# Kernel tuning notes

Measured on AMD Instinct MI355X. Metric: run time of the kernel, lower is better.

## Reference

```python
import jax, jax.numpy as jnp
import numpy as np

# static config (matches init_kwargs)
E = 1280          # n_embed
L = 4             # n_layer
NH = 16           # n_heads
D = E // NH       # head_dim = 80
M = 5120          # n_mlp
O = 2048          # n_output_embed
MS = 2            # spatial_merge_size
NGPS = 48         # sqrt(num_position_embeddings)
GRID_T, GRID_H, GRID_W = 1, 32, 32
N_IMG = 2
SPP = GRID_T * GRID_H * GRID_W   # 1024 tokens per image
S = N_IMG * SPP                  # 2048 total tokens
H4 = E * MS * MS                 # merger hidden = 5120
IN_PATCH = 3 * 2 * 16 * 16       # 1536
DS_IDX = [1, 2]


def _ln(x, w, b, eps=1e-6):
    m = x.mean(-1, keepdims=True)
    v = ((x - m) ** 2).mean(-1, keepdims=True)
    return (x - m) / jnp.sqrt(v + eps) * w + b


def _pos_embed_interp(pos_emb):
    # bilinear interpolation of the 48x48 learned grid to GRID_HxGRID_W, per image
    hi = jnp.linspace(0.0, NGPS - 1.0, GRID_H)
    wi = jnp.linspace(0.0, NGPS - 1.0, GRID_W)
    hf = hi.astype(jnp.int32); wf = wi.astype(jnp.int32)
    hc = jnp.minimum(hf + 1, NGPS - 1); wc = jnp.minimum(wf + 1, NGPS - 1)
    dh = hi - hf; dw = wi - wf
    idx = [(hf[:, None] * NGPS + wf[None]).ravel(), (hf[:, None] * NGPS + wc[None]).ravel(),
           (hc[:, None] * NGPS + wf[None]).ravel(), (hc[:, None] * NGPS + wc[None]).ravel()]
    wts = [((1 - dh)[:, None] * (1 - dw)[None]).ravel(), ((1 - dh)[:, None] * dw[None]).ravel(),
           (dh[:, None] * (1 - dw)[None]).ravel(), (dh[:, None] * dw[None]).ravel()]
    pe = sum(pos_emb[i] * w[:, None] for i, w in zip(idx, wts))  # [h*w, E]
    pe = jnp.tile(pe, (GRID_T, 1))
    # spatial-merge permutation: (t, h/m, m, w/m, m) -> (t, h/m, w/m, m, m)
    pe = pe.reshape(GRID_T, GRID_H // MS, MS, GRID_W // MS, MS, E).transpose(0, 1, 3, 2, 4, 5).reshape(-1, E)
    return jnp.tile(pe, (N_IMG, 1))  # [S, E]


def _rotary_freqs():
    dim = D // 2  # VisionRotaryEmbedding dim = 40
    inv = 1.0 / (10000.0 ** (jnp.arange(0, dim, 2, dtype=jnp.float32) / dim))  # [D//4]
    hp = jnp.broadcast_to(jnp.arange(GRID_H)[:, None], (GRID_H, GRID_W))
    hp = hp.reshape(GRID_H // MS, MS, GRID_W // MS, MS).transpose(0, 2, 1, 3).ravel()
    wp = jnp.broadcast_to(jnp.arange(GRID_W)[None, :], (GRID_H, GRID_W))
    wp = wp.reshape(GRID_H // MS, MS, GRID_W // MS, MS).transpose(0, 2, 1, 3).ravel()
    pos = jnp.stack([hp, wp], -1)            # [h*w, 2]
    pos = jnp.tile(pos, (GRID_T, 1))
    pos = jnp.tile(pos, (N_IMG, 1))          # [S, 2]
    table = jnp.arange(max(GRID_H, GRID_W), dtype=jnp.float32)[:, None] * inv[None]  # [G, D//4]
    return table[pos].reshape(S, -1)         # [S, D//2] (h-freqs || w-freqs)


def _rope(t, cos, sin):
    # t: [S, NH, D]; cos/sin: [S, 1, D]; applied in float32 as in the source
    t1, t2 = jnp.split(t, 2, axis=-1)
    rot = jnp.concatenate([-t2, t1], -1)
    return (t.astype(jnp.float32) * cos + rot.astype(jnp.float32) * sin).astype(t.dtype)


def _attn(x, qkv_w, qkv_b, pw, pb, cos, sin, mask):
    qkv = (x @ qkv_w.T + qkv_b).reshape(S, 3, NH, D)
    q, k, v = qkv[:, 0], qkv[:, 1], qkv[:, 2]
    q = _rope(q, cos, sin)
    k = _rope(k, cos, sin)
    scores = jnp.einsum('shd,thd->hst', q, k) / np.sqrt(D).astype(np.float32) + mask
    p = jax.nn.softmax(scores.astype(jnp.float32), axis=-1).astype(q.dtype)
    o = jnp.einsum('hst,thd->shd', p, v).reshape(S, E)
    return o @ pw.T + pb


def _merger(x, ln_w, ln_b, f1w, f1b, f2w, f2b, post):
    if post:
        x = _ln(x.reshape(-1, H4), ln_w, ln_b)
    else:
        x = _ln(x, ln_w, ln_b).reshape(-1, H4)
    h = jax.nn.gelu(x @ f1w.T + f1b, approximate=False)  # nn.GELU() exact
    return h @ f2w.T + f2b


def setup_inputs() -> dict:
    key = jax.random.key(0)
    ks = iter(jax.random.split(key, 24))
    n = lambda s: jax.random.normal(next(ks), s, dtype=jnp.float32) * 0.02
    return {
        'x': jax.random.normal(next(ks), (S, IN_PATCH), dtype=jnp.float32),
        'patch_w': n((E, IN_PATCH)), 'patch_b': jnp.zeros((E,), jnp.float32),
        'pos_emb': n((NGPS * NGPS, E)),
        'ln1_w': jnp.ones((L, E), jnp.float32), 'ln1_b': jnp.zeros((L, E), jnp.float32),
        'ln2_w': jnp.ones((L, E), jnp.float32), 'ln2_b': jnp.zeros((L, E), jnp.float32),
        'qkv_w': n((L, 3 * E, E)), 'qkv_b': jnp.zeros((L, 3 * E), jnp.float32),
        'attn_proj_w': n((L, E, E)), 'attn_proj_b': jnp.zeros((L, E), jnp.float32),
        'fc1_w': n((L, M, E)), 'fc1_b': jnp.zeros((L, M), jnp.float32),
        'fc2_w': n((L, E, M)), 'fc2_b': jnp.zeros((L, E), jnp.float32),
        'm_ln_w': jnp.ones((E,), jnp.float32), 'm_ln_b': jnp.zeros((E,), jnp.float32),
        'm_fc1_w': n((H4, H4)), 'm_fc1_b': jnp.zeros((H4,), jnp.float32),
        'm_fc2_w': n((O, H4)), 'm_fc2_b': jnp.zeros((O,), jnp.float32),
        'ds_ln_w': jnp.ones((2, H4), jnp.float32), 'ds_ln_b': jnp.zeros((2, H4), jnp.float32),
        'ds_fc1_w': n((2, H4, H4)), 'ds_fc1_b': jnp.zeros((2, H4), jnp.float32),
        'ds_fc2_w': n((2, O, H4)), 'ds_fc2_b': jnp.zeros((2, O), jnp.float32),
    }


def reference(x, patch_w, patch_b, pos_emb, ln1_w, ln1_b, ln2_w, ln2_b,
              qkv_w, qkv_b, attn_proj_w, attn_proj_b, fc1_w, fc1_b, fc2_w, fc2_b,
              m_ln_w, m_ln_b, m_fc1_w, m_fc1_b, m_fc2_w, m_fc2_b,
              ds_ln_w, ds_ln_b, ds_fc1_w, ds_fc1_b, ds_fc2_w, ds_fc2_b):
    # patch embed (Conv3d with kernel==stride == per-patch linear)
    h = x @ patch_w.T + patch_b                      # [S, E]
    h = h + _pos_embed_interp(pos_emb)
    freqs = _rotary_freqs()                          # [S, D//2]
    cos = jnp.concatenate([jnp.cos(freqs)] * 2, -1)[:, None, :]  # [S,1,D]
    sin = jnp.concatenate([jnp.sin(freqs)] * 2, -1)[:, None, :]
    img = jnp.arange(S) // SPP                       # cu_seqlens block-diagonal mask
    mask = jnp.where(img[:, None] == img[None, :], 0.0, jnp.finfo(jnp.float32).min)
    ds_feats = []
    for l in range(L):
        h = h + _attn(_ln(h, ln1_w[l], ln1_b[l]), qkv_w[l], qkv_b[l],
                      attn_proj_w[l], attn_proj_b[l], cos, sin, mask)
        hn = _ln(h, ln2_w[l], ln2_b[l])
        h = h + (jax.nn.gelu(hn @ fc1_w[l].T + fc1_b[l], approximate=True) @ fc2_w[l].T + fc2_b[l])
        if l in DS_IDX:
            j = DS_IDX.index(l)
            ds_feats.append(_merger(h, ds_ln_w[j], ds_ln_b[j], ds_fc1_w[j], ds_fc1_b[j],
                                    ds_fc2_w[j], ds_fc2_b[j], post=True))
    main = _merger(h, m_ln_w, m_ln_b, m_fc1_w, m_fc1_b, m_fc2_w, m_fc2_b, post=False)
    return jnp.stack([main] + ds_feats, 0)           # [3, S//4, O]
```

## Files before the change

kernel.cpp:

```cpp
#include <hip/hip_runtime.h>
#include <hip/hip_bf16.h>
#include <cstdio>
#include <cstdint>

#define E_    1280
#define L_    4
#define NH_   16
#define D_    80
#define DP_   96
#define MLP_  5120
#define O_    2048
#define S_    2048
#define H4_   5120
#define INP_  1536

typedef __attribute__((ext_vector_type(4))) float f32x4;
typedef __attribute__((ext_vector_type(8))) short short8v;
typedef __attribute__((ext_vector_type(4))) short short4v;

__device__ __forceinline__ short f2bf(float f){
  uint32_t u = __float_as_uint(f);
  uint32_t r = (u + 0x7FFFu + ((u >> 16) & 1u)) >> 16;
  return (short)r;
}
__device__ __forceinline__ float bf2f(short s){
  return __uint_as_float(((uint32_t)(uint16_t)s) << 16);
}
__device__ __forceinline__ float gelu_tanh(float x){
  const float z = 0.7978845608028654f*(x + 0.044715f*x*x*x);
  const float e = __expf(2.f*z);
  return 0.5f*x*(1.f + (e-1.f)/(e+1.f));
}
__device__ __forceinline__ float gelu_erf(float x){
  return 0.5f*x*(1.f + erff(x*0.7071067811865476f));
}
__device__ __forceinline__ void token_hw(int t, int& hc, int& wc){
  hc = ((t>>1)&1) + ((t>>6)<<1);
  wc = (t&1)      + (((t>>2)&15)<<1);
}

__device__ __forceinline__ void gload16(const short* g, short* l){
  __builtin_amdgcn_global_load_lds((const __attribute__((address_space(1))) void*)g,
                                   (__attribute__((address_space(3))) void*)l, 16, 0, 0);
}

__global__ __launch_bounds__(256)
void cvt_k(const float* __restrict__ src, short* __restrict__ dst, long long n)
{
  const long long stride = (long long)gridDim.x*256*8;
  for (long long i = ((long long)blockIdx.x*256 + threadIdx.x)*8; i < n; i += stride){
    float4 v0 = *(const float4*)(src+i);
    float4 v1 = *(const float4*)(src+i+4);
    short8v w;
    w[0]=f2bf(v0.x); w[1]=f2bf(v0.y); w[2]=f2bf(v0.z); w[3]=f2bf(v0.w);
    w[4]=f2bf(v1.x); w[5]=f2bf(v1.y); w[6]=f2bf(v1.z); w[7]=f2bf(v1.w);
    *(short8v*)(dst+i) = w;
  }
}

struct Gemm2P {
  const short* A; const short* B; void* C;
  const float* bias;
  short* part;
  int lda, ldb, ldc, M, N, K;
  float scale;
  long long aOffH, aOffI, bOffH, bOffI, cOffH, cOffI;
  int nImg, kSplit;
};

template<int EPI, bool RES, bool CF32, bool SPLIT>
__global__ __launch_bounds__(256)
void gemm2_k(Gemm2P p)
{
  __shared__ short As[3][4096];
  __shared__ short Bs[3][4096];

  int z = blockIdx.z, ks = 0;
  if constexpr (SPLIT){ ks = z % p.kSplit; z /= p.kSplit; }
  const int hI = z / p.nImg, iI = z % p.nImg;
  const long long aB = (long long)hI*p.aOffH + (long long)iI*p.aOffI;
  const long long bB = (long long)hI*p.bOffH + (long long)iI*p.bOffI;
  const long long cB = (long long)hI*p.cOffH + (long long)iI*p.cOffI;

  const int nwg = gridDim.x*gridDim.y;
  const int orig = blockIdx.y*gridDim.x + blockIdx.x;
  const int q8 = nwg >> 3, r8 = nwg & 7;
  const int xcd = orig & 7, oidx = orig >> 3;
  const int wg = (xcd < r8 ? xcd*(q8+1) : r8*(q8+1) + (xcd-r8)*q8) + oidx;
  const int nt = wg % gridDim.x, mt = wg / gridDim.x;

  const int tid = threadIdx.x, lane = tid & 63, wv = tid >> 6;

  const int sr = lane >> 2;
  const int sc = (lane & 3) * 8;
  const int Kp  = SPLIT ? p.K / p.kSplit : p.K;
  const int kBeg = SPLIT ? ks * Kp : 0;
  int ra0 = mt*128 + (wv*2+0)*16 + sr; if (ra0 >= p.M) ra0 = p.M-1;
  int ra1 = mt*128 + (wv*2+1)*16 + sr; if (ra1 >= p.M) ra1 = p.M-1;
  int rb0 = nt*128 + (wv*2+0)*16 + sr; if (rb0 >= p.N) rb0 = p.N-1;
  int rb1 = nt*128 + (wv*2+1)*16 + sr; if (rb1 >= p.N) rb1 = p.N-1;
  const short* pa0 = p.A + aB + (long long)ra0*p.lda + sc + kBeg;
  const short* pa1 = p.A + aB + (long long)ra1*p.lda + sc + kBeg;
  const short* pb0 = p.B + bB + (long long)rb0*p.ldb + sc + kBeg;
  const short* pb1 = p.B + bB + (long long)rb1*p.ldb + sc + kBeg;
  const int so0 = (wv*2+0)*512;
  const int so1 = (wv*2+1)*512;

  const int fr = lane & 15, fo = (lane >> 4) * 8;
  const int wr = (wv >> 1) * 64, wc = (wv & 1) * 64;

  f32x4 acc[4][4] = {};

  auto stage = [&](int buf, int t){
    const int k0 = t << 5;
    gload16(pa0 + k0, &As[buf][so0]);
    gload16(pa1 + k0, &As[buf][so1]);
    gload16(pb0 + k0, &Bs[buf][so0]);
    gload16(pb1 + k0, &Bs[buf][so1]);
  };

  const int ntile = Kp >> 5;
  stage(0, 0);
  if (ntile > 1) stage(1, 1);
  for (int t = 0; t < ntile; t++){
    const int cur = t % 3;
    if (t + 1 < ntile) { asm volatile("s_waitcnt vmcnt(4)" ::: "memory"); }
    else               { asm volatile("s_waitcnt vmcnt(0)" ::: "memory"); }
    __builtin_amdgcn_s_barrier();
    asm volatile("" ::: "memory");
    short8v a[4], b[4];
    #pragma unroll
    for (int i=0;i<4;i++){
      a[i] = *(const short8v*)&As[cur][(wr + i*16 + fr)*32 + fo];
      b[i] = *(const short8v*)&Bs[cur][(wc + i*16 + fr)*32 + fo];
    }
    if (t + 2 < ntile) stage((t+2)%3, t+2);
    #pragma unroll
    for (int i=0;i<4;i++)
      #pragma unroll
      for (int j=0;j<4;j++)
        acc[i][j] = __builtin_amdgcn_mfma_f32_16x16x32_bf16(a[i], b[j], acc[i][j], 0, 0, 0);
  }

  #pragma unroll
  for (int i=0;i<4;i++){
    #pragma unroll
    for (int j=0;j<4;j++){
      #pragma unroll
      for (int r=0;r<4;r++){
        const int row = mt*128 + wr + i*16 + (lane>>4)*4 + r;
        const int col = nt*128 + wc + j*16 + fr;
        if (row < p.M && col < p.N){
          float v = acc[i][j][r];
          if constexpr (SPLIT){
            p.part[((long long)ks*p.M + row)*p.N + col] = f2bf(v);
          } else {
            if (p.bias) v += p.bias[col];
            if constexpr (EPI==1) v = gelu_tanh(v);
            if constexpr (EPI==2) v = gelu_erf(v);
            if constexpr (EPI==3) v *= p.scale;
            const long long off = cB + (long long)row*p.ldc + col;
            if constexpr (RES)  v += ((const float*)p.C)[off];
            if constexpr (CF32) ((float*)p.C)[off] = v;
            else                ((short*)p.C)[off] = f2bf(v);
          }
        }
      }
    }
  }
}

template<int EPI, bool RES, bool CF32>
__global__ __launch_bounds__(256)
void reduce_k(const short* __restrict__ part, int kSplit, long long MN, int N,
              const float* __restrict__ bias, void* __restrict__ C)
{
  const long long i = ((long long)blockIdx.x*256 + threadIdx.x)*8;
  if (i >= MN) return;
  float v[8];
  { short8v pv = *(const short8v*)(part + i);
    #pragma unroll
    for (int e=0;e<8;e++) v[e] = bf2f(pv[e]); }
  for (int ks = 1; ks < kSplit; ks++){
    short8v pv = *(const short8v*)(part + (long long)ks*MN + i);
    #pragma unroll
    for (int e=0;e<8;e++) v[e] += bf2f(pv[e]);
  }
  if (bias){
    const int col = (int)(i % N);
    #pragma unroll
    for (int e=0;e<8;e++) v[e] += bias[col+e];
  }
  #pragma unroll
  for (int e=0;e<8;e++){
    if constexpr (EPI==1) v[e] = gelu_tanh(v[e]);
    if constexpr (EPI==2) v[e] = gelu_erf(v[e]);
  }
  if constexpr (RES){
    const float* cp = (const float*)C + i;
    #pragma unroll
    for (int e=0;e<8;e++) v[e] += cp[e];
  }
  if constexpr (CF32){
    float4 o0 = {v[0],v[1],v[2],v[3]}, o1 = {v[4],v[5],v[6],v[7]};
    *(float4*)((float*)C + i) = o0;
    *(float4*)((float*)C + i + 4) = o1;
  } else {
    short8v o;
    #pragma unroll
    for (int e=0;e<8;e++) o[e] = f2bf(v[e]);
    *(short8v*)((short*)C + i) = o;
  }
}

__global__ __launch_bounds__(256)
void redln_k(const short* __restrict__ part, long long MN, const float* __restrict__ bias,
             float* __restrict__ h, const float* __restrict__ lnw, const float* __restrict__ lnb,
             short* __restrict__ aln)
{
  __shared__ float red[8];
  const int row = blockIdx.x, tid = threadIdx.x;
  float4 vals[2];
  float s = 0.f, sq = 0.f;
  #pragma unroll
  for (int it=0; it<2; it++){
    const int c = tid*4 + it*1024;
    if (c < E_){
      float4 v = *(const float4*)(h + (long long)row*E_ + c);
      const float4 b = *(const float4*)(bias + c);
      v.x += b.x; v.y += b.y; v.z += b.z; v.w += b.w;
      #pragma unroll
      for (int ks=0; ks<4; ks++){
        short4v pv = *(const short4v*)(part + (long long)ks*MN + (long long)row*E_ + c);
        v.x += bf2f(pv[0]); v.y += bf2f(pv[1]); v.z += bf2f(pv[2]); v.w += bf2f(pv[3]);
      }
      *(float4*)(h + (long long)row*E_ + c) = v;
      vals[it] = v;
      s  += v.x+v.y+v.z+v.w;
      sq += v.x*v.x+v.y*v.y+v.z*v.z+v.w*v.w;
    }
  }
  #pragma unroll
  for (int m=32;m;m>>=1){ s += __shfl_xor(s,m,64); sq += __shfl_xor(sq,m,64); }
  const int wv = tid>>6, lane = tid&63;
  if (lane==0){ red[wv]=s; red[4+wv]=sq; }
  __syncthreads();
  s  = red[0]+red[1]+red[2]+red[3];
  sq = red[4]+red[5]+red[6]+red[7];
  const float mean = s / (float)E_;
  const float var  = sq / (float)E_ - mean*mean;
  const float rs   = rsqrtf(var + 1e-6f);
  #pragma unroll
  for (int it=0; it<2; it++){
    const int c = tid*4 + it*1024;
    if (c < E_){
      const float4 v = vals[it];
      const float4 gw = *(const float4*)(lnw + c);
      const float4 bw = *(const float4*)(lnb + c);
      short4v o;
      o[0] = f2bf((v.x-mean)*rs*gw.x + bw.x);
      o[1] = f2bf((v.y-mean)*rs*gw.y + bw.y);
      o[2] = f2bf((v.z-mean)*rs*gw.z + bw.z);
      o[3] = f2bf((v.w-mean)*rs*gw.w + bw.w);
      *(short4v*)(aln + (long long)row*E_ + c) = o;
    }
  }
}

__global__ __launch_bounds__(256)
void redposln_k(const short* __restrict__ part, long long MN, const float* __restrict__ bias,
                const float* __restrict__ pe, float* __restrict__ h,
                const float* __restrict__ lnw, const float* __restrict__ lnb,
                short* __restrict__ aln)
{
  __shared__ float red[8];
  const int row = blockIdx.x, tid = threadIdx.x;
  const int t = row & 1023;
  int hc, wc; token_hw(t, hc, wc);
  const float hi = (float)hc * (47.f/31.f);
  const float wi = (float)wc * (47.f/31.f);
  int hf = (int)hi; float dh = hi - (float)hf; int h2 = min(hf+1, 47);
  int wf = (int)wi; float dw = wi - (float)wf; int w2 = min(wf+1, 47);
  const float w00=(1.f-dh)*(1.f-dw), w01=(1.f-dh)*dw, w10=dh*(1.f-dw), w11=dh*dw;
  const float* pe00 = pe + (long long)(hf*48+wf)*E_;
  const float* pe01 = pe + (long long)(hf*48+w2)*E_;
  const float* pe10 = pe + (long long)(h2*48+wf)*E_;
  const float* pe11 = pe + (long long)(h2*48+w2)*E_;

  float4 vals[2];
  float s = 0.f, sq = 0.f;
  #pragma unroll
  for (int it=0; it<2; it++){
    const int c = tid*4 + it*1024;
    if (c < E_){
      const float4 b = *(const float4*)(bias + c);
      const float4 a0 = *(const float4*)(pe00 + c);
      const float4 a1 = *(const float4*)(pe01 + c);
      const float4 a2 = *(const float4*)(pe10 + c);
      const float4 a3 = *(const float4*)(pe11 + c);
      float4 v;
      v.x = b.x + w00*a0.x + w01*a1.x + w10*a2.x + w11*a3.x;
      v.y = b.y + w00*a0.y + w01*a1.y + w10*a2.y + w11*a3.y;
      v.z = b.z + w00*a0.z + w01*a1.z + w10*a2.z + w11*a3.z;
      v.w = b.w + w00*a0.w + w01*a1.w + w10*a2.w + w11*a3.w;
      #pragma unroll
      for (int ks=0; ks<4; ks++){
        short4v pv = *(const short4v*)(part + (long long)ks*MN + (long long)row*E_ + c);
        v.x += bf2f(pv[0]); v.y += bf2f(pv[1]); v.z += bf2f(pv[2]); v.w += bf2f(pv[3]);
      }
      *(float4*)(h + (long long)row*E_ + c) = v;
      vals[it] = v;
      s  += v.x+v.y+v.z+v.w;
      sq += v.x*v.x+v.y*v.y+v.z*v.z+v.w*v.w;
    }
  }
  #pragma unroll
  for (int m=32;m;m>>=1){ s += __shfl_xor(s,m,64); sq += __shfl_xor(sq,m,64); }
  const int wv = tid>>6, lane = tid&63;
  if (lane==0){ red[wv]=s; red[4+wv]=sq; }
  __syncthreads();
  s  = red[0]+red[1]+red[2]+red[3];
  sq = red[4]+red[5]+red[6]+red[7];
  const float mean = s / (float)E_;
  const float var  = sq / (float)E_ - mean*mean;
  const float rs   = rsqrtf(var + 1e-6f);
  #pragma unroll
  for (int it=0; it<2; it++){
    const int c = tid*4 + it*1024;
    if (c < E_){
      const float4 v = vals[it];
      const float4 gw = *(const float4*)(lnw + c);
      const float4 bw = *(const float4*)(lnb + c);
      short4v o;
      o[0] = f2bf((v.x-mean)*rs*gw.x + bw.x);
      o[1] = f2bf((v.y-mean)*rs*gw.y + bw.y);
      o[2] = f2bf((v.z-mean)*rs*gw.z + bw.z);
      o[3] = f2bf((v.w-mean)*rs*gw.w + bw.w);
      *(short4v*)(aln + (long long)row*E_ + c) = o;
    }
  }
}

__global__ __launch_bounds__(256)
void fattn_k(const short* __restrict__ qh, const short* __restrict__ kh,
             const short* __restrict__ vt, short* __restrict__ o2)
{
  __shared__ short Ps[4][16*136];

  const int qt = blockIdx.x, h = blockIdx.y, img = blockIdx.z;
  const int tid = threadIdx.x, lane = tid & 63, wv = tid >> 6;
  const int fr = lane & 15, fo = (lane >> 4) * 8, g = lane >> 4;

  const short* qp = qh + ((long long)h*S_ + img*1024 + qt*64 + wv*16)*DP_;
  const short* kp = kh + ((long long)h*S_ + img*1024)*DP_;
  const short* vp = vt + ((long long)(h*2 + img))*80*1024;
  short* Pw = &Ps[wv][0];

  short8v q[3];
  #pragma unroll
  for (int t3=0;t3<3;t3++)
    q[t3] = *(const short8v*)(qp + (long long)fr*DP_ + t3*32 + fo);

  float m_[4], l_[4];
  f32x4 ao[5] = {};
  #pragma unroll
  for (int r=0;r<4;r++){ m_[r] = -3.0e38f; l_[r] = 0.f; }

  for (int t = 0; t < 8; t++){
    f32x4 sc[8] = {};
    #pragma unroll
    for (int j=0;j<8;j++){
      #pragma unroll
      for (int t3=0;t3<3;t3++){
        const short8v kb = *(const short8v*)(kp + (long long)(t*128 + j*16 + fr)*DP_ + t3*32 + fo);
        sc[j] = __builtin_amdgcn_mfma_f32_16x16x32_bf16(q[t3], kb, sc[j], 0,0,0);
      }
    }
    #pragma unroll
    for (int j=0;j<8;j++) sc[j] *= 0.11180339887498949f;

    #pragma unroll
    for (int r=0;r<4;r++){
      float mx = sc[0][r];
      #pragma unroll
      for (int j=1;j<8;j++) mx = fmaxf(mx, sc[j][r]);
      mx = fmaxf(mx, __shfl_xor(mx, 1, 64));
      mx = fmaxf(mx, __shfl_xor(mx, 2, 64));
      mx = fmaxf(mx, __shfl_xor(mx, 4, 64));
      mx = fmaxf(mx, __shfl_xor(mx, 8, 64));
      const float mn = fmaxf(m_[r], mx);
      const float al = __expf(m_[r] - mn);
      float ts = 0.f;
      #pragma unroll
      for (int j=0;j<8;j++){
        const float pv = __expf(sc[j][r] - mn);
        sc[j][r] = pv;
        ts += pv;
      }
      ts += __shfl_xor(ts, 1, 64);
      ts += __shfl_xor(ts, 2, 64);
      ts += __shfl_xor(ts, 4, 64);
      ts += __shfl_xor(ts, 8, 64);
      l_[r] = l_[r]*al + ts;
      m_[r] = mn;
      #pragma unroll
      for (int n=0;n<5;n++) ao[n][r] *= al;
      const int prow = g*4 + r;
      #pragma unroll
      for (int j=0;j<8;j++) Pw[prow*136 + j*16 + fr] = f2bf(sc[j][r]);
    }
    asm volatile("s_waitcnt lgkmcnt(0)" ::: "memory");
    __builtin_amdgcn_sched_barrier(0);

    #pragma unroll
    for (int t4=0;t4<4;t4++){
      const short8v pa = *(const short8v*)&Pw[fr*136 + t4*32 + fo];
      #pragma unroll
      for (int n=0;n<5;n++){
        const short8v vb = *(const short8v*)(vp + (long long)(n*16 + fr)*1024 + t*128 + t4*32 + fo);
        ao[n] = __builtin_amdgcn_mfma_f32_16x16x32_bf16(pa, vb, ao[n], 0,0,0);
      }
    }
  }

  short* op = o2 + ((long long)(img*1024 + qt*64 + wv*16))*E_ + h*80;
  #pragma unroll
  for (int r=0;r<4;r++){
    const float inv = 1.f / l_[r];
    const int row = g*4 + r;
    #pragma unroll
    for (int n=0;n<5;n++)
      op[(long long)row*E_ + n*16 + fr] = f2bf(ao[n][r] * inv);
  }
}

__global__ __launch_bounds__(256)
void ln_k(const float* __restrict__ X, const float* __restrict__ g, const float* __restrict__ bta,
          short* __restrict__ Y, int Cn)
{
  __shared__ float red[8];
  const int row = blockIdx.x;
  const float* x = X + (long long)row*Cn;
  short* y = Y + (long long)row*Cn;
  float s = 0.f, sq = 0.f;
  for (int c = threadIdx.x*4; c < Cn; c += 1024){
    float4 v = *(const float4*)(x + c);
    s  += v.x+v.y+v.z+v.w;
    sq += v.x*v.x+v.y*v.y+v.z*v.z+v.w*v.w;
  }
  #pragma unroll
  for (int m=32;m;m>>=1){ s += __shfl_xor(s,m,64); sq += __shfl_xor(sq,m,64); }
  const int wv = threadIdx.x>>6, lane = threadIdx.x&63;
  if (lane==0){ red[wv]=s; red[4+wv]=sq; }
  __syncthreads();
  s  = red[0]+red[1]+red[2]+red[3];
  sq = red[4]+red[5]+red[6]+red[7];
  const float mean = s / (float)Cn;
  const float var  = sq / (float)Cn - mean*mean;
  const float rs   = rsqrtf(var + 1e-6f);
  for (int c = threadIdx.x*4; c < Cn; c += 1024){
    float4 v  = *(const float4*)(x + c);
    float4 gw = *(const float4*)(g + c);
    float4 bw = *(const float4*)(bta + c);
    short4v o;
    o[0] = f2bf((v.x-mean)*rs*gw.x + bw.x);
    o[1] = f2bf((v.y-mean)*rs*gw.y + bw.y);
    o[2] = f2bf((v.z-mean)*rs*gw.z + bw.z);
    o[3] = f2bf((v.w-mean)*rs*gw.w + bw.w);
    *(short4v*)(y + c) = o;
  }
}

__global__ __launch_bounds__(256)
void rope_k(const short* __restrict__ qkv, short* __restrict__ qh,
            short* __restrict__ kh, short* __restrict__ vt)
{
  const int idx = blockIdx.x*256 + threadIdx.x;
  if (idx >= S_*NH_*40) return;
  const int d0 = idx % 40;
  const int h  = (idx / 40) % NH_;
  const int s  = idx / (40*NH_);
  const int t  = s & 1023, img = s >> 10;
  int hc, wc; token_hw(t, hc, wc);
  const int j  = d0 % 20;
  const float invf = exp2f(-0.66438561897747f * (float)j);
  const float pos  = (float)((d0 < 20) ? hc : wc);
  float sn, cs;
  __sincosf(pos * invf, &sn, &cs);
  const short* base = qkv + (long long)s*3840 + h*80;
  const float q1 = bf2f(base[d0]),      q2 = bf2f(base[d0+40]);
  const float k1 = bf2f(base[1280+d0]), k2 = bf2f(base[1280+d0+40]);
  const long long qo = ((long long)h*S_ + s)*DP_;
  qh[qo + d0]    = f2bf(q1*cs - q2*sn);
  qh[qo + d0+40] = f2bf(q2*cs + q1*sn);
  kh[qo + d0]    = f2bf(k1*cs - k2*sn);
  kh[qo + d0+40] = f2bf(k2*cs + k1*sn);
  if (d0 < 16){ qh[qo + 80 + d0] = 0; kh[qo + 80 + d0] = 0; }
  const long long vo = (((long long)h*2 + img)*80)*1024 + t;
  vt[vo + (long long)d0*1024]      = base[2560+d0];
  vt[vo + (long long)(d0+40)*1024] = base[2560+d0+40];
}

static Gemm2P mk(const short* A, const short* B, void* C, const float* bias,
                 int lda, int ldb, int ldc, int M, int N, int K, float scale = 1.f)
{
  Gemm2P p{}; p.A=A; p.B=B; p.C=C; p.bias=bias; p.part=nullptr;
  p.lda=lda; p.ldb=ldb; p.ldc=ldc; p.M=M; p.N=N; p.K=K; p.scale=scale;
  p.aOffH=p.aOffI=p.bOffH=p.bOffI=p.cOffH=p.cOffI=0; p.nImg=1; p.kSplit=1;
  return p;
}

extern "C" void kernel_launch(void* const* d_in, const int* in_sizes, int n_in,
                              void* d_out, int out_size, void* d_ws, size_t ws_size,
                              hipStream_t stream)
{
  const float* x           = (const float*)d_in[0];
  const float* patch_w     = (const float*)d_in[1];
  const float* patch_b     = (const float*)d_in[2];
  const float* pos_emb     = (const float*)d_in[3];
  const float* ln1_w       = (const float*)d_in[4];
  const float* ln1_b       = (const float*)d_in[5];
  const float* ln2_w       = (const float*)d_in[6];
  const float* ln2_b       = (const float*)d_in[7];
  const float* qkv_w       = (const float*)d_in[8];
  const float* qkv_b       = (const float*)d_in[9];
  const float* attn_proj_w = (const float*)d_in[10];
  const float* attn_proj_b = (const float*)d_in[11];
  const float* fc1_w       = (const float*)d_in[12];
  const float* fc1_b       = (const float*)d_in[13];
  const float* fc2_w       = (const float*)d_in[14];
  const float* fc2_b       = (const float*)d_in[15];
  const float* m_ln_w      = (const float*)d_in[16];
  const float* m_ln_b      = (const float*)d_in[17];
  const float* m_fc1_w     = (const float*)d_in[18];
  const float* m_fc1_b     = (const float*)d_in[19];
  const float* m_fc2_w     = (const float*)d_in[20];
  const float* m_fc2_b     = (const float*)d_in[21];
  const float* ds_ln_w     = (const float*)d_in[22];
  const float* ds_ln_b     = (const float*)d_in[23];
  const float* ds_fc1_w    = (const float*)d_in[24];
  const float* ds_fc1_b    = (const float*)d_in[25];
  const float* ds_fc2_w    = (const float*)d_in[26];
  const float* ds_fc2_b    = (const float*)d_in[27];
  float* out = (float*)d_out;

  char* wsp = (char*)d_ws;
  auto alloc = [&](size_t bytes)->char*{
    char* p = wsp; wsp += (bytes + 255) & ~(size_t)255; return p;
  };
  float* h    = (float*)alloc((size_t)S_*E_*4);
  short* qkvb = (short*)alloc((size_t)S_*3840*2);
  short* aln  = (short*)alloc((size_t)S_*E_*2);
  short* qh   = (short*)alloc((size_t)NH_*S_*DP_*2);
  short* kh   = (short*)alloc((size_t)NH_*S_*DP_*2 + 4096);
  short* vt   = (short*)alloc((size_t)NH_*2*D_*1024*2 + 4096);
  short* part = (short*)alloc((size_t)48*1024*1024);
  short* o2   = (short*)alloc((size_t)S_*E_*2);
  short* ffn  = (short*)alloc((size_t)S_*MLP_*2);
  short* xb    = (short*)alloc((size_t)S_*INP_*2);
  short* pwB   = (short*)alloc((size_t)E_*INP_*2);
  short* qkvwB = (short*)alloc((size_t)L_*3840*E_*2);
  short* prwB  = (short*)alloc((size_t)L_*E_*E_*2);
  short* f1wB  = (short*)alloc((size_t)L_*MLP_*E_*2);
  short* f2wB  = (short*)alloc((size_t)L_*E_*MLP_*2);
  short* mf1B  = (short*)alloc((size_t)H4_*H4_*2);
  short* mf2B  = (short*)alloc((size_t)O_*H4_*2);
  short* df1B  = (short*)alloc((size_t)2*H4_*H4_*2);
  short* df2B  = (short*)alloc((size_t)2*O_*H4_*2);
  size_t need = (size_t)(wsp - (char*)d_ws);
  if (need > ws_size){
    fprintf(stderr, "kernel_launch: ws too small: need %zu have %zu\n", need, ws_size);
    return;
  }
  short* dsln = qkvb;

  const dim3 B256(256);
  auto cvt = [&](const float* src, short* dst, long long n){
    unsigned blk = (unsigned)min((long long)8192, (n/8 + 255)/256);
    cvt_k<<<blk, B256, 0, stream>>>(src, dst, n);
  };
  cvt(x, xb, (long long)S_*INP_);
  cvt(patch_w, pwB, (long long)E_*INP_);
  cvt(qkv_w, qkvwB, (long long)L_*3840*E_);
  cvt(attn_proj_w, prwB, (long long)L_*E_*E_);
  cvt(fc1_w, f1wB, (long long)L_*MLP_*E_);
  cvt(fc2_w, f2wB, (long long)L_*E_*MLP_);
  cvt(m_fc1_w, mf1B, (long long)H4_*H4_);
  cvt(m_fc2_w, mf2B, (long long)O_*H4_);
  cvt(ds_fc1_w, df1B, (long long)2*H4_*H4_);
  cvt(ds_fc2_w, df2B, (long long)2*O_*H4_);

  auto G = [](int M, int N, int ks = 1){
    return dim3((unsigned)((N+127)/128), (unsigned)((M+127)/128), (unsigned)ks);
  };
  auto RG = [](long long MN){ return dim3((unsigned)((MN/8 + 255)/256)); };

  { Gemm2P pp = mk(xb, pwB, nullptr, nullptr, INP_, INP_, E_, S_, E_, INP_);
    pp.part = part; pp.kSplit = 4;
    gemm2_k<0,false,true,true><<<G(S_,E_,4),B256,0,stream>>>(pp);
    redposln_k<<<S_, B256, 0, stream>>>(part, (long long)S_*E_, patch_b, pos_emb,
                                        h, ln1_w, ln1_b, aln); }

  for (int l = 0; l < L_; l++){
    { Gemm2P pp = mk(aln, qkvwB + (size_t)l*3840*E_, qkvb, qkv_b + l*3840, E_, E_, 3840, S_, 3840, E_);
      gemm2_k<0,false,false,false><<<G(S_,3840),B256,0,stream>>>(pp); }
    rope_k<<<(S_*NH_*40+255)/256, B256, 0, stream>>>(qkvb, qh, kh, vt);
    fattn_k<<<dim3(16,16,2), B256, 0, stream>>>(qh, kh, vt, o2);
    { Gemm2P pp = mk(o2, prwB + (size_t)l*E_*E_, nullptr, nullptr, E_, E_, E_, S_, E_, E_);
      pp.part = part; pp.kSplit = 4;
      gemm2_k<0,false,true,true><<<G(S_,E_,4),B256,0,stream>>>(pp);
      redln_k<<<S_, B256, 0, stream>>>(part, (long long)S_*E_, attn_proj_b + l*E_,
                                       h, ln2_w + l*E_, ln2_b + l*E_, aln); }

    { Gemm2P pp = mk(aln, f1wB + (size_t)l*MLP_*E_, ffn, fc1_b + l*MLP_, E_, E_, MLP_, S_, MLP_, E_);
      gemm2_k<1,false,false,false><<<G(S_,MLP_),B256,0,stream>>>(pp); }
    { Gemm2P pp = mk(ffn, f2wB + (size_t)l*E_*MLP_, nullptr, nullptr, MLP_, MLP_, E_, S_, E_, MLP_);
      pp.part = part; pp.kSplit = 4;
      gemm2_k<0,false,true,true><<<G(S_,E_,4),B256,0,stream>>>(pp);
      const float* nw = (l < 3) ? (ln1_w + (l+1)*E_) : m_ln_w;
      const float* nb = (l < 3) ? (ln1_b + (l+1)*E_) : m_ln_b;
      redln_k<<<S_, B256, 0, stream>>>(part, (long long)S_*E_, fc2_b + l*E_, h, nw, nb, aln); }

    if (l == 1 || l == 2){
      const int j = l - 1;
      ln_k<<<512, B256, 0, stream>>>(h, ds_ln_w + (size_t)j*H4_, ds_ln_b + (size_t)j*H4_, dsln, H4_);
      { Gemm2P pp = mk(dsln, df1B + (size_t)j*H4_*H4_, ffn, nullptr, H4_, H4_, H4_, 512, H4_, H4_);
        pp.part = part; pp.kSplit = 4;
        gemm2_k<0,false,false,true><<<G(512,H4_,4),B256,0,stream>>>(pp);
        reduce_k<2,false,false><<<RG((long long)512*H4_),B256,0,stream>>>(part, 4, (long long)512*H4_, H4_, ds_fc1_b + (size_t)j*H4_, ffn); }
      { Gemm2P pp = mk(ffn, df2B + (size_t)j*O_*H4_, out + (size_t)(1+j)*512*O_, nullptr, H4_, H4_, O_, 512, O_, H4_);
        pp.part = part; pp.kSplit = 8;
        gemm2_k<0,false,true,true><<<G(512,O_,8),B256,0,stream>>>(pp);
        reduce_k<0,false,true><<<RG((long long)512*O_),B256,0,stream>>>(part, 8, (long long)512*O_, O_, ds_fc2_b + (size_t)j*O_, out + (size_t)(1+j)*512*O_); }
    }
  }

  { Gemm2P pp = mk(aln, mf1B, ffn, nullptr, H4_, H4_, H4_, 512, H4_, H4_);
    pp.part = part; pp.kSplit = 4;
    gemm2_k<0,false,false,true><<<G(512,H4_,4),B256,0,stream>>>(pp);
    reduce_k<2,false,false><<<RG((long long)512*H4_),B256,0,stream>>>(part, 4, (long long)512*H4_, H4_, m_fc1_b, ffn); }
  { Gemm2P pp = mk(ffn, mf2B, out, nullptr, H4_, H4_, O_, 512, O_, H4_);
    pp.part = part; pp.kSplit = 8;
    gemm2_k<0,false,true,true><<<G(512,O_,8),B256,0,stream>>>(pp);
    reduce_k<0,false,true><<<RG((long long)512*O_),B256,0,stream>>>(part, 8, (long long)512*O_, O_, m_fc2_b, out); }
}
```

Before: 1.688 ms.

## Replace GEMM with 256x256-tile 8-wave split-K kernel using swizzled LDS

Replaces the 128x128 triple-buffered GEMM with a 512-thread kernel that computes 256x256 output tiles. It uses a K-step of 64, XOR-swizzled LDS layout, double buffering and a four-phase load/compute interleave with s_setprio. All GEMMs now go through split-K with a separate reduce pass, including QKV and FC1, whose bias and GELU epilogues move into reduce_k. This is meant to raise data reuse per tile and cut LDS bank conflicts. In exchange it adds extra partial-sum traffic and reduce launches for the formerly fused GEMMs, and it assumes M and N are multiples of 256.

```diff
diff --git a/kernel.cpp b/kernel.cpp
--- a/kernel.cpp
+++ b/kernel.cpp
@@ -38,7 +38,6 @@
   hc = ((t>>1)&1) + ((t>>6)<<1);
   wc = (t&1)      + (((t>>2)&15)<<1);
 }
-
 __device__ __forceinline__ void gload16(const short* g, short* l){
   __builtin_amdgcn_global_load_lds((const __attribute__((address_space(1))) void*)g,
                                    (__attribute__((address_space(3))) void*)l, 16, 0, 0);
@@ -58,29 +57,21 @@
   }
 }
 
-struct Gemm2P {
-  const short* A; const short* B; void* C;
-  const float* bias;
-  short* part;
-  int lda, ldb, ldc, M, N, K;
-  float scale;
-  long long aOffH, aOffI, bOffH, bOffI, cOffH, cOffI;
-  int nImg, kSplit;
+struct G8P {
+  const short* A; const short* B; short* part;
+  int lda, ldb, M, N, K, kSplit;
 };
 
-template<int EPI, bool RES, bool CF32, bool SPLIT>
-__global__ __launch_bounds__(256)
-void gemm2_k(Gemm2P p)
-{
-  __shared__ short As[3][4096];
-  __shared__ short Bs[3][4096];
-
-  int z = blockIdx.z, ks = 0;
-  if constexpr (SPLIT){ ks = z % p.kSplit; z /= p.kSplit; }
-  const int hI = z / p.nImg, iI = z % p.nImg;
-  const long long aB = (long long)hI*p.aOffH + (long long)iI*p.aOffI;
-  const long long bB = (long long)hI*p.bOffH + (long long)iI*p.bOffI;
-  const long long cB = (long long)hI*p.cOffH + (long long)iI*p.cOffI;
+__global__ __launch_bounds__(512, 2)
+void g8_k(G8P p)
+{
+  __shared__ short Ab[2][2][8192];
+  __shared__ short Bb[2][2][8192];
+
+  const int ks  = blockIdx.z;
+  const int Kp  = p.K / p.kSplit;
+  const int kBeg = ks * Kp;
+  const int NT  = Kp >> 6;
 
   const int nwg = gridDim.x*gridDim.y;
   const int orig = blockIdx.y*gridDim.x + blockIdx.x;
@@ -90,84 +81,108 @@
   const int nt = wg % gridDim.x, mt = wg / gridDim.x;
 
   const int tid = threadIdx.x, lane = tid & 63, wv = tid >> 6;
-
-  const int sr = lane >> 2;
-  const int sc = (lane & 3) * 8;
-  const int Kp  = SPLIT ? p.K / p.kSplit : p.K;
-  const int kBeg = SPLIT ? ks * Kp : 0;
-  int ra0 = mt*128 + (wv*2+0)*16 + sr; if (ra0 >= p.M) ra0 = p.M-1;
-  int ra1 = mt*128 + (wv*2+1)*16 + sr; if (ra1 >= p.M) ra1 = p.M-1;
-  int rb0 = nt*128 + (wv*2+0)*16 + sr; if (rb0 >= p.N) rb0 = p.N-1;
-  int rb1 = nt*128 + (wv*2+1)*16 + sr; if (rb1 >= p.N) rb1 = p.N-1;
-  const short* pa0 = p.A + aB + (long long)ra0*p.lda + sc + kBeg;
-  const short* pa1 = p.A + aB + (long long)ra1*p.lda + sc + kBeg;
-  const short* pb0 = p.B + bB + (long long)rb0*p.ldb + sc + kBeg;
-  const short* pb1 = p.B + bB + (long long)rb1*p.ldb + sc + kBeg;
-  const int so0 = (wv*2+0)*512;
-  const int so1 = (wv*2+1)*512;
-
-  const int fr = lane & 15, fo = (lane >> 4) * 8;
-  const int wr = (wv >> 1) * 64, wc = (wv & 1) * 64;
-
-  f32x4 acc[4][4] = {};
-
-  auto stage = [&](int buf, int t){
-    const int k0 = t << 5;
-    gload16(pa0 + k0, &As[buf][so0]);
-    gload16(pa1 + k0, &As[buf][so1]);
-    gload16(pb0 + k0, &Bs[buf][so0]);
-    gload16(pb1 + k0, &Bs[buf][so1]);
+  const int qm = wv >> 2, qn = wv & 3, fr = lane & 15, g4 = lane >> 4;
+
+  int sRow[2], sCol[2];
+  #pragma unroll
+  for (int ld=0; ld<2; ld++){
+    const int off = ld*8192 + tid*16;
+    const int r = off >> 7, cb = off & 127;
+    sRow[ld] = r;
+    sCol[ld] = (cb ^ ((r&7)<<4)) >> 1;
+  }
+  const short* Agl = p.A + (size_t)(mt*256)*p.lda + kBeg;
+  const short* Bgl = p.B + (size_t)(nt*256)*p.ldb + kBeg;
+
+  auto stA = [&](int buf, int hf, int ktn){
+    #pragma unroll
+    for (int ld=0; ld<2; ld++)
+      gload16(Agl + (size_t)(hf*128 + sRow[ld])*p.lda + ktn*64 + sCol[ld],
+              &Ab[buf][hf][0] + ld*4096 + wv*512);
   };
-
-  const int ntile = Kp >> 5;
-  stage(0, 0);
-  if (ntile > 1) stage(1, 1);
-  for (int t = 0; t < ntile; t++){
-    const int cur = t % 3;
-    if (t + 1 < ntile) { asm volatile("s_waitcnt vmcnt(4)" ::: "memory"); }
-    else               { asm volatile("s_waitcnt vmcnt(0)" ::: "memory"); }
-    __builtin_amdgcn_s_barrier();
-    asm volatile("" ::: "memory");
-    short8v a[4], b[4];
-    #pragma unroll
-    for (int i=0;i<4;i++){
-      a[i] = *(const short8v*)&As[cur][(wr + i*16 + fr)*32 + fo];
-      b[i] = *(const short8v*)&Bs[cur][(wc + i*16 + fr)*32 + fo];
-    }
-    if (t + 2 < ntile) stage((t+2)%3, t+2);
-    #pragma unroll
-    for (int i=0;i<4;i++)
-      #pragma unroll
-      for (int j=0;j<4;j++)
-        acc[i][j] = __builtin_amdgcn_mfma_f32_16x16x32_bf16(a[i], b[j], acc[i][j], 0, 0, 0);
-  }
-
-  #pragma unroll
-  for (int i=0;i<4;i++){
-    #pragma unroll
-    for (int j=0;j<4;j++){
-      #pragma unroll
-      for (int r=0;r<4;r++){
-        const int row = mt*128 + wr + i*16 + (lane>>4)*4 + r;
-        const int col = nt*128 + wc + j*16 + fr;
-        if (row < p.M && col < p.N){
-          float v = acc[i][j][r];
-          if constexpr (SPLIT){
-            p.part[((long long)ks*p.M + row)*p.N + col] = f2bf(v);
-          } else {
-            if (p.bias) v += p.bias[col];
-            if constexpr (EPI==1) v = gelu_tanh(v);
-            if constexpr (EPI==2) v = gelu_erf(v);
-            if constexpr (EPI==3) v *= p.scale;
-            const long long off = cB + (long long)row*p.ldc + col;
-            if constexpr (RES)  v += ((const float*)p.C)[off];
-            if constexpr (CF32) ((float*)p.C)[off] = v;
-            else                ((short*)p.C)[off] = f2bf(v);
+  auto stB = [&](int buf, int hf, int ktn){
+    #pragma unroll
+    for (int ld=0; ld<2; ld++)
+      gload16(Bgl + (size_t)(hf*128 + sRow[ld])*p.ldb + ktn*64 + sCol[ld],
+              &Bb[buf][hf][0] + ld*4096 + wv*512);
+  };
+
+  f32x4 acc[2][2][4][2] = {};
+
+  stA(0,0,0); stB(0,0,0); stB(0,1,0); stA(0,1,0);
+
+  for (int kt = 0; kt < NT; ++kt){
+    const int cur = kt & 1;
+    const bool more = (kt + 1 < NT);
+    #pragma unroll
+    for (int ph = 0; ph < 4; ++ph){
+      const int rh = ph >> 1, ch = ph & 1;
+      if (ph == 0){ asm volatile("s_waitcnt vmcnt(4)" ::: "memory"); }
+      else if (ph == 1){
+        if (more) asm volatile("s_waitcnt vmcnt(4)" ::: "memory");
+        else      asm volatile("s_waitcnt vmcnt(2)" ::: "memory");
+      } else if (ph == 2){
+        if (more) asm volatile("s_waitcnt vmcnt(4)" ::: "memory");
+        else      asm volatile("s_waitcnt vmcnt(0)" ::: "memory");
+      }
+      __builtin_amdgcn_s_barrier();
+      __builtin_amdgcn_sched_barrier(0);
+
+      short8v a[4][2], b[2][2];
+      #pragma unroll
+      for (int i=0;i<4;i++){
+        const int rA = qm*64 + i*16 + fr;
+        #pragma unroll
+        for (int kb=0;kb<2;kb++){
+          const int col = ((kb*64 + g4*16) ^ ((rA&7)<<4)) >> 1;
+          a[i][kb] = *(const short8v*)&Ab[cur][rh][rA*64 + col];
+        }
+      }
+      #pragma unroll
+      for (int j=0;j<2;j++){
+        const int rB = qn*32 + j*16 + fr;
+        #pragma unroll
+        for (int kb=0;kb<2;kb++){
+          const int col = ((kb*64 + g4*16) ^ ((rB&7)<<4)) >> 1;
+          b[j][kb] = *(const short8v*)&Bb[cur][ch][rB*64 + col];
+        }
+      }
+      if (more){
+        if      (ph == 0) stA(cur^1, 0, kt+1);
+        else if (ph == 1) stB(cur^1, 0, kt+1);
+        else if (ph == 2) stB(cur^1, 1, kt+1);
+        else              stA(cur^1, 1, kt+1);
+      }
+      asm volatile("s_waitcnt lgkmcnt(0)" ::: "memory");
+      __builtin_amdgcn_sched_barrier(0);
+      __builtin_amdgcn_s_setprio(1);
+      #pragma unroll
+      for (int kb=0;kb<2;kb++)
+        #pragma unroll
+        for (int i=0;i<4;i++)
+          #pragma unroll
+          for (int j=0;j<2;j++)
+            acc[rh][ch][i][j] = __builtin_amdgcn_mfma_f32_16x16x32_bf16(
+                                  a[i][kb], b[j][kb], acc[rh][ch][i][j], 0,0,0);
+      __builtin_amdgcn_s_setprio(0);
+    }
+  }
+
+  short* pp = p.part + (size_t)ks*p.M*p.N;
+  #pragma unroll
+  for (int rh=0;rh<2;rh++)
+    #pragma unroll
+    for (int ch=0;ch<2;ch++)
+      #pragma unroll
+      for (int i=0;i<4;i++)
+        #pragma unroll
+        for (int j=0;j<2;j++)
+          #pragma unroll
+          for (int r4=0;r4<4;r4++){
+            const int row = mt*256 + rh*128 + qm*64 + i*16 + g4*4 + r4;
+            const int col = nt*256 + ch*128 + qn*32 + j*16 + fr;
+            pp[(size_t)row*p.N + col] = f2bf(acc[rh][ch][i][j][r4]);
           }
-        }
-      }
-    }
-  }
 }
 
 template<int EPI, bool RES, bool CF32>
@@ -499,15 +514,6 @@
   const long long vo = (((long long)h*2 + img)*80)*1024 + t;
   vt[vo + (long long)d0*1024]      = base[2560+d0];
   vt[vo + (long long)(d0+40)*1024] = base[2560+d0+40];
-}
-
-static Gemm2P mk(const short* A, const short* B, void* C, const float* bias,
-                 int lda, int ldb, int ldc, int M, int N, int K, float scale = 1.f)
-{
-  Gemm2P p{}; p.A=A; p.B=B; p.C=C; p.bias=bias; p.part=nullptr;
-  p.lda=lda; p.ldb=ldb; p.ldc=ldc; p.M=M; p.N=N; p.K=K; p.scale=scale;
-  p.aOffH=p.aOffI=p.bOffH=p.bOffI=p.cOffH=p.cOffI=0; p.nImg=1; p.kSplit=1;
-  return p;
 }
 
 extern "C" void kernel_launch(void* const* d_in, const int* in_sizes, int n_in,
@@ -574,7 +580,7 @@
   }
   short* dsln = qkvb;
 
-  const dim3 B256(256);
+  const dim3 B256(256), B512(512);
   auto cvt = [&](const float* src, short* dst, long long n){
     unsigned blk = (unsigned)min((long long)8192, (n/8 + 255)/256);
     cvt_k<<<blk, B256, 0, stream>>>(src, dst, n);
@@ -590,57 +596,44 @@
   cvt(ds_fc1_w, df1B, (long long)2*H4_*H4_);
   cvt(ds_fc2_w, df2B, (long long)2*O_*H4_);
 
-  auto G = [](int M, int N, int ks = 1){
-    return dim3((unsigned)((N+127)/128), (unsigned)((M+127)/128), (unsigned)ks);
+  auto g8 = [&](const short* A, const short* B, int lda, int ldb,
+                int M, int N, int K, int kSplit){
+    G8P p{A, B, part, lda, ldb, M, N, K, kSplit};
+    g8_k<<<dim3((unsigned)(N/256), (unsigned)(M/256), (unsigned)kSplit), B512, 0, stream>>>(p);
   };
   auto RG = [](long long MN){ return dim3((unsigned)((MN/8 + 255)/256)); };
 
-  { Gemm2P pp = mk(xb, pwB, nullptr, nullptr, INP_, INP_, E_, S_, E_, INP_);
-    pp.part = part; pp.kSplit = 4;
-    gemm2_k<0,false,true,true><<<G(S_,E_,4),B256,0,stream>>>(pp);
-    redposln_k<<<S_, B256, 0, stream>>>(part, (long long)S_*E_, patch_b, pos_emb,
-                                        h, ln1_w, ln1_b, aln); }
+  g8(xb, pwB, INP_, INP_, S_, E_, INP_, 4);
+  redposln_k<<<S_, B256, 0, stream>>>(part, (long long)S_*E_, patch_b, pos_emb,
+                                      h, ln1_w, ln1_b, aln);
 
   for (int l = 0; l < L_; l++){
-    { Gemm2P pp = mk(aln, qkvwB + (size_t)l*3840*E_, qkvb, qkv_b + l*3840, E_, E_, 3840, S_, 3840, E_);
-      gemm2_k<0,false,false,false><<<G(S_,3840),B256,0,stream>>>(pp); }
+    g8(aln, qkvwB + (size_t)l*3840*E_, E_, E_, S_, 3840, E_, 2);
+    reduce_k<0,false,false><<<RG((long long)S_*3840),B256,0,stream>>>(part, 2, (long long)S_*3840, 3840, qkv_b + l*3840, qkvb);
     rope_k<<<(S_*NH_*40+255)/256, B256, 0, stream>>>(qkvb, qh, kh, vt);
     fattn_k<<<dim3(16,16,2), B256, 0, stream>>>(qh, kh, vt, o2);
-    { Gemm2P pp = mk(o2, prwB + (size_t)l*E_*E_, nullptr, nullptr, E_, E_, E_, S_, E_, E_);
-      pp.part = part; pp.kSplit = 4;
-      gemm2_k<0,false,true,true><<<G(S_,E_,4),B256,0,stream>>>(pp);
-      redln_k<<<S_, B256, 0, stream>>>(part, (long long)S_*E_, attn_proj_b + l*E_,
-                                       h, ln2_w + l*E_, ln2_b + l*E_, aln); }
-
-    { Gemm2P pp = mk(aln, f1wB + (size_t)l*MLP_*E_, ffn, fc1_b + l*MLP_, E_, E_, MLP_, S_, MLP_, E_);
-      gemm2_k<1,false,false,false><<<G(S_,MLP_),B256,0,stream>>>(pp); }
-    { Gemm2P pp = mk(ffn, f2wB + (size_t)l*E_*MLP_, nullptr, nullptr, MLP_, MLP_, E_, S_, E_, MLP_);
-      pp.part = part; pp.kSplit = 4;
-      gemm2_k<0,false,true,true><<<G(S_,E_,4),B256,0,stream>>>(pp);
-      const float* nw = (l < 3) ? (ln1_w + (l+1)*E_) : m_ln_w;
-      const float* nb = (l < 3) ? (ln1_b + (l+1)*E_) : m_ln_b;
-      redln_k<<<S_, B256, 0, stream>>>(part, (long long)S_*E_, fc2_b + l*E_, h, nw, nb, aln); }
+    g8(o2, prwB + (size_t)l*E_*E_, E_, E_, S_, E_, E_, 4);
+    redln_k<<<S_, B256, 0, stream>>>(part, (long long)S_*E_, attn_proj_b + l*E_,
+                                     h, ln2_w + l*E_, ln2_b + l*E_, aln);
+    g8(aln, f1wB + (size_t)l*MLP_*E_, E_, E_, S_, MLP_, E_, 2);
+    reduce_k<1,false,false><<<RG((long long)S_*MLP_),B256,0,stream>>>(part, 2, (long long)S_*MLP_, MLP_, fc1_b + l*MLP_, ffn);
+    g8(ffn, f2wB + (size_t)l*E_*MLP_, MLP_, MLP_, S_, E_, MLP_, 4);
+    const float* nw = (l < 3) ? (ln1_w + (l+1)*E_) : m_ln_w;
+    const float* nb = (l < 3) ? (ln1_b + (l+1)*E_) : m_ln_b;
+    redln_k<<<S_, B256, 0, stream>>>(part, (long long)S_*E_, fc2_b + l*E_, h, nw, nb, aln);
 
     if (l == 1 || l == 2){
       const int j = l - 1;
       ln_k<<<512, B256, 0, stream>>>(h, ds_ln_w + (size_t)j*H4_, ds_ln_b + (size_t)j*H4_, dsln, H4_);
-      { Gemm2P pp = mk(dsln, df1B + (size_t)j*H4_*H4_, ffn, nullptr, H4_, H4_, H4_, 512, H4_, H4_);
-        pp.part = part; pp.kSplit = 4;
-        gemm2_k<0,false,false,true><<<G(512,H4_,4),B256,0,stream>>>(pp);
-        reduce_k<2,false,false><<<RG((long long)512*H4_),B256,0,stream>>>(part, 4, (long long)512*H4_, H4_, ds_fc1_b + (size_t)j*H4_, ffn); }
-      { Gemm2P pp = mk(ffn, df2B + (size_t)j*O_*H4_, out + (size_t)(1+j)*512*O_, nullptr, H4_, H4_, O_, 512, O_, H4_);
-        pp.part = part; pp.kSplit = 8;
-        gemm2_k<0,false,true,true><<<G(512,O_,8),B256,0,stream>>>(pp);
-        reduce_k<0,false,true><<<RG((long long)512*O_),B256,0,stream>>>(part, 8, (long long)512*O_, O_, ds_fc2_b + (size_t)j*O_, out + (size_t)(1+j)*512*O_); }
-    }
-  }
-
-  { Gemm2P pp = mk(aln, mf1B, ffn, nullptr, H4_, H4_, H4_, 512, H4_, H4_);
-    pp.part = part; pp.kSplit = 4;
-    gemm2_k<0,false,false,true><<<G(512,H4_,4),B256,0,stream>>>(pp);
-    reduce_k<2,false,false><<<RG((long long)512*H4_),B256,0,stream>>>(part, 4, (long long)512*H4_, H4_, m_fc1_b, ffn); }
-  { Gemm2P pp = mk(ffn, mf2B, out, nullptr, H4_, H4_, O_, 512, O_, H4_);
-    pp.part = part; pp.kSplit = 8;
-    gemm2_k<0,false,true,true><<<G(512,O_,8),B256,0,stream>>>(pp);
-    reduce_k<0,false,true><<<RG((long long)512*O_),B256,0,stream>>>(part, 8, (long long)512*O_, O_, m_fc2_b, out); }
-}
+      g8(dsln, df1B + (size_t)j*H4_*H4_, H4_, H4_, 512, H4_, H4_, 4);
+      reduce_k<2,false,false><<<RG((long long)512*H4_),B256,0,stream>>>(part, 4, (long long)512*H4_, H4_, ds_fc1_b + (size_t)j*H4_, ffn);
+      g8(ffn, df2B + (size_t)j*O_*H4_, H4_, H4_, 512, O_, H4_, 8);
+      reduce_k<0,false,true><<<RG((long long)512*O_),B256,0,stream>>>(part, 8, (long long)512*O_, O_, ds_fc2_b + (size_t)j*O_, out + (size_t)(1+j)*512*O_);
+    }
+  }
+
+  g8(aln, mf1B, H4_, H4_, 512, H4_, H4_, 4);
+  reduce_k<2,false,false><<<RG((long long)512*H4_),B256,0,stream>>>(part, 4, (long long)512*H4_, H4_, m_fc1_b, ffn);
+  g8(ffn, mf2B, H4_, H4_, 512, O_, H4_, 8);
+  reduce_k<0,false,true><<<RG((long long)512*O_),B256,0,stream>>>(part, 8, (long long)512*O_, O_, m_fc2_b, out);
+}
```

Result: slower. 1.793 ms (+6.2%).
